# Performance work log

Hardware: AMD Instinct MI355X
Metric: run time of the kernel (lower is better)

Reference implementation:

```python
import jax, jax.numpy as jnp
from jax import lax
import numpy as np

D_IN, D_MODEL, N_CLS, NL = 63, 256, 14, 4
D_INNER, D_STATE, NH, HP, DCONV = 512, 128, 8, 64, 4
CONV_CH = D_INNER + 2 * D_STATE  # 768
PROJ = 2 * D_INNER + 2 * D_STATE + NH  # 1288
EPS = 1e-5


def layernorm(x, w, b):
    mu = jnp.mean(x, -1, keepdims=True)
    var = jnp.mean((x - mu) ** 2, -1, keepdims=True)
    return (x - mu) * lax.rsqrt(var + EPS) * w + b


def mamba2_block(u, inproj_w, conv_w, conv_b, dt_bias, A_log, Dp, norm_w, outp_w):
    B, L, _ = u.shape
    zxbcdt = u @ inproj_w.T  # (B,L,1288)
    z = zxbcdt[..., :D_INNER]
    xBC = zxbcdt[..., D_INNER:D_INNER + CONV_CH]
    dt = zxbcdt[..., D_INNER + CONV_CH:]  # (B,L,NH)
    # depthwise causal conv1d, kernel 4
    xp = jnp.pad(xBC, ((0, 0), (DCONV - 1, 0), (0, 0)))
    conv = conv_b + sum(xp[:, k:k + L, :] * conv_w[k] for k in range(DCONV))
    xBC = jax.nn.silu(conv)
    xs = xBC[..., :D_INNER].reshape(B, L, NH, HP)
    Bm = xBC[..., D_INNER:D_INNER + D_STATE]  # (B,L,N)
    Cm = xBC[..., D_INNER + D_STATE:]
    dt = jax.nn.softplus(dt + dt_bias)  # (B,L,NH)
    A = -jnp.exp(A_log)  # (NH,)
    dA = jnp.exp(dt * A)  # (B,L,NH)
    dtx = dt[..., None] * xs  # (B,L,NH,HP)

    def step(h, inp):
        dA_t, dtx_t, B_t, C_t = inp
        h = h * dA_t[:, :, None, None] + jnp.einsum('bhp,bn->bhpn', dtx_t, B_t)
        y = jnp.einsum('bhpn,bn->bhp', h, C_t)
        return h, y

    h0 = jnp.zeros((B, NH, HP, D_STATE), u.dtype)
    _, ys = lax.scan(step, h0, (dA.transpose(1, 0, 2), dtx.transpose(1, 0, 2, 3),
                                 Bm.transpose(1, 0, 2), Cm.transpose(1, 0, 2)))
    y = ys.transpose(1, 0, 2, 3) + Dp[None, None, :, None] * xs  # (B,L,NH,HP)
    y = y.reshape(B, L, D_INNER)
    g = y * jax.nn.silu(z)  # gated RMSNorm (norm_before_gate=False)
    g = g * lax.rsqrt(jnp.mean(g * g, -1, keepdims=True) + EPS) * norm_w
    return g @ outp_w.T


def setup_inputs() -> dict:
    key = jax.random.key(0)
    ks = jax.random.split(key, 20)
    B, L = 32, 1024
    s = 0.02
    inp = {
        'x': jax.random.normal(ks[0], (B, L, D_IN), jnp.float32),
        'in_w': jax.random.normal(ks[1], (D_MODEL, D_IN)) * s,
        'in_b': jnp.zeros((D_MODEL,)),
        'lnin_w': jnp.ones((D_MODEL,)),
        'lnin_b': jnp.zeros((D_MODEL,)),
        'inproj_w': jax.random.normal(ks[2], (NL, PROJ, D_MODEL)) * s,
        'conv_w': jax.random.normal(ks[3], (NL, DCONV, CONV_CH)) * 0.1,
        'conv_b': jnp.zeros((NL, CONV_CH)),
        'dt_bias': jax.random.uniform(ks[4], (NL, NH), minval=-4.0, maxval=-1.0),
        'A_log': jnp.log(jax.random.uniform(ks[5], (NL, NH), minval=1.0, maxval=16.0)),
        'D': jnp.ones((NL, NH)),
        'norm_w': jnp.ones((NL, D_INNER)),
        'outp_w': jax.random.normal(ks[6], (NL, D_MODEL, D_INNER)) * s,
        'ln_w': jnp.ones((NL, D_MODEL)),
        'ln_b': jnp.zeros((NL, D_MODEL)),
        'head_w': jax.random.normal(ks[7], (N_CLS, D_MODEL)) * s,
        'head_b': jnp.zeros((N_CLS,)),
        'lengths': jax.random.randint(ks[8], (B,), 1, L + 1, dtype=jnp.int32),
    }
    return inp


def reference(x, in_w, in_b, lnin_w, lnin_b, inproj_w, conv_w, conv_b, dt_bias,
              A_log, D, norm_w, outp_w, ln_w, ln_b, head_w, head_b, lengths):
    B, L, _ = x.shape
    h = layernorm(x @ in_w.T + in_b, lnin_w, lnin_b)
    for i in range(NL):
        res = h
        m = mamba2_block(h, inproj_w[i], conv_w[i], conv_b[i], dt_bias[i],
                         A_log[i], D[i], norm_w[i], outp_w[i])
        h = layernorm(m + res, ln_w[i], ln_b[i])
    mask = (jnp.arange(L)[None, :] < lengths[:, None]).astype(h.dtype)[:, :, None]
    pooled = jnp.sum(h * mask, axis=1) / lengths[:, None].astype(h.dtype)
    return pooled @ head_w.T + head_b
```

## Files before the change

### kernel.cpp

```cpp
#include <hip/hip_runtime.h>
#include <math.h>

#define D_IN 63
#define D_MODEL 256
#define N_CLS 14
#define NL 4
#define D_INNER 512
#define D_STATE 128
#define NH 8
#define HP 64
#define DCONV 4
#define CONV_CH 768
#define PROJ 1288
#define XBCDT 776
#define EPS 1e-5f
#define BSZ 32
#define LSEQ 1024
#define NTOK (BSZ*LSEQ)

#define SSEG 4
#define TSEG (LSEQ/SSEG)
#define CT 16

typedef __attribute__((ext_vector_type(8))) short bf16x8;
typedef __attribute__((ext_vector_type(4))) float f32x4;

__device__ __forceinline__ float silu_f(float x) { return x / (1.f + expf(-x)); }

__device__ __forceinline__ unsigned short f2bf(float x) {
    union { float f; unsigned u; } v; v.f = x;
    unsigned r = v.u + 0x7FFFu + ((v.u >> 16) & 1u);
    return (unsigned short)(r >> 16);
}
__device__ __forceinline__ float bf2f(unsigned short h) {
    union { float f; unsigned u; } v; v.u = ((unsigned)h) << 16; return v.f;
}

__device__ __forceinline__ int swz128(int n) {
    int q = n >> 5, i = (n >> 2) & 7, j = n & 3;
    return (q << 5) + (((i + 2 * q) & 7) << 2) + j;
}

__device__ __forceinline__ float2 block_reduce2(float a, float b, float* sred) {
    #pragma unroll
    for (int off = 32; off >= 1; off >>= 1) {
        a += __shfl_xor(a, off);
        b += __shfl_xor(b, off);
    }
    int wid = threadIdx.x >> 6, lane = threadIdx.x & 63;
    if (lane == 0) { sred[wid * 2] = a; sred[wid * 2 + 1] = b; }
    __syncthreads();
    a = sred[0] + sred[2] + sred[4] + sred[6];
    b = sred[1] + sred[3] + sred[5] + sred[7];
    __syncthreads();
    return make_float2(a, b);
}

#define LDKP 40
__global__ __launch_bounds__(256, 2)
void k_gemm_mfma(const float* __restrict__ A, const float* __restrict__ B,
                 float* __restrict__ C, int M, int N, int K) {
    __shared__ unsigned short Ah[128][LDKP], Al[128][LDKP];
    __shared__ unsigned short Bh[128][LDKP], Bl[128][LDKP];
    int n0 = blockIdx.x * 128, m0 = blockIdx.y * 128;
    int tid = threadIdx.x;
    int srow = tid >> 1, sk = (tid & 1) * 16;
    int lane = tid & 63, wave = tid >> 6;
    int wm = (wave >> 1) * 64, wn = (wave & 1) * 64;
    int ln = lane & 15, quad = lane >> 4;
    f32x4 acc[4][4];
    #pragma unroll
    for (int i = 0; i < 4; i++)
        #pragma unroll
        for (int j = 0; j < 4; j++) acc[i][j] = (f32x4){0.f, 0.f, 0.f, 0.f};
    const float* Ap = A + (size_t)(m0 + srow) * K + sk;
    const float* Bp = B + (size_t)(n0 + srow) * K + sk;
    bool bval = (n0 + srow) < N;
    for (int k0 = 0; k0 < K; k0 += 32) {
        float av[16], bv[16];
        #pragma unroll
        for (int i = 0; i < 4; i++) {
            *(float4*)&av[4 * i] = *(const float4*)(Ap + k0 + 4 * i);
            *(float4*)&bv[4 * i] = bval ? *(const float4*)(Bp + k0 + 4 * i)
                                        : make_float4(0.f, 0.f, 0.f, 0.f);
        }
        __syncthreads();
        #pragma unroll
        for (int g = 0; g < 2; g++) {
            unsigned hiA[4], loA[4], hiB[4], loB[4];
            #pragma unroll
            for (int j = 0; j < 4; j++) {
                float a0 = av[8 * g + 2 * j], a1 = av[8 * g + 2 * j + 1];
                unsigned short h0 = f2bf(a0), h1 = f2bf(a1);
                unsigned short l0 = f2bf(a0 - bf2f(h0)), l1 = f2bf(a1 - bf2f(h1));
                hiA[j] = (unsigned)h0 | ((unsigned)h1 << 16);
                loA[j] = (unsigned)l0 | ((unsigned)l1 << 16);
                float b0 = bv[8 * g + 2 * j], b1 = bv[8 * g + 2 * j + 1];
                unsigned short g0 = f2bf(b0), g1 = f2bf(b1);
                unsigned short m0s = f2bf(b0 - bf2f(g0)), m1s = f2bf(b1 - bf2f(g1));
                hiB[j] = (unsigned)g0 | ((unsigned)g1 << 16);
                loB[j] = (unsigned)m0s | ((unsigned)m1s << 16);
            }
            *(uint4*)&Ah[srow][sk + 8 * g] = *(uint4*)hiA;
            *(uint4*)&Al[srow][sk + 8 * g] = *(uint4*)loA;
            *(uint4*)&Bh[srow][sk + 8 * g] = *(uint4*)hiB;
            *(uint4*)&Bl[srow][sk + 8 * g] = *(uint4*)loB;
        }
        __syncthreads();
        bf16x8 fah[4], fal[4], fbh[4], fbl[4];
        #pragma unroll
        for (int t = 0; t < 4; t++) {
            fah[t] = *(const bf16x8*)&Ah[wm + t * 16 + ln][quad * 8];
            fal[t] = *(const bf16x8*)&Al[wm + t * 16 + ln][quad * 8];
            fbh[t] = *(const bf16x8*)&Bh[wn + t * 16 + ln][quad * 8];
            fbl[t] = *(const bf16x8*)&Bl[wn + t * 16 + ln][quad * 8];
        }
        #pragma unroll
        for (int mt = 0; mt < 4; mt++)
            #pragma unroll
            for (int nt = 0; nt < 4; nt++) {
                acc[mt][nt] = __builtin_amdgcn_mfma_f32_16x16x32_bf16(fal[mt], fbh[nt], acc[mt][nt], 0, 0, 0);
                acc[mt][nt] = __builtin_amdgcn_mfma_f32_16x16x32_bf16(fah[mt], fbl[nt], acc[mt][nt], 0, 0, 0);
                acc[mt][nt] = __builtin_amdgcn_mfma_f32_16x16x32_bf16(fah[mt], fbh[nt], acc[mt][nt], 0, 0, 0);
            }
    }
    #pragma unroll
    for (int mt = 0; mt < 4; mt++)
        #pragma unroll
        for (int nt = 0; nt < 4; nt++) {
            int cn = n0 + wn + nt * 16 + ln;
            if (cn < N) {
                #pragma unroll
                for (int r = 0; r < 4; r++) {
                    int cm = m0 + wm + mt * 16 + quad * 4 + r;
                    C[(size_t)cm * N + cn] = acc[mt][nt][r];
                }
            }
        }
}

__global__ __launch_bounds__(256)
void k_pack_x(const float* __restrict__ x, float* __restrict__ xp) {
    size_t idx = (size_t)blockIdx.x * 256 + threadIdx.x;
    int k = (int)(idx & 63);
    size_t m = idx >> 6;
    xp[idx] = (k < D_IN) ? x[m * D_IN + k] : 0.f;
}
__global__ __launch_bounds__(256)
void k_pack_w(const float* __restrict__ w, float* __restrict__ wp) {
    int idx = blockIdx.x * 256 + threadIdx.x;
    int k = idx & 63, n = idx >> 6;
    wp[idx] = (k < D_IN) ? w[n * D_IN + k] : 0.f;
}

__global__ __launch_bounds__(256)
void k_lnio(const float* __restrict__ pre, const float* __restrict__ bias,
            const float* __restrict__ gw, const float* __restrict__ gb,
            float* __restrict__ h) {
    int m = blockIdx.x, o = threadIdx.x;
    __shared__ float sred[8];
    float v = pre[(size_t)m * D_MODEL + o] + bias[o];
    float2 s = block_reduce2(v, v * v, sred);
    float mu = s.x * (1.f / D_MODEL);
    float var = s.y * (1.f / D_MODEL) - mu * mu;
    h[(size_t)m * D_MODEL + o] = (v - mu) * rsqrtf(var + EPS) * gw[o] + gb[o];
}

__global__ __launch_bounds__(256)
void k_conv(const float* __restrict__ xbc, const float* __restrict__ cw,
            const float* __restrict__ cb, const float* __restrict__ dtb,
            float* __restrict__ xs, float* __restrict__ Bm, float* __restrict__ Cm,
            float* __restrict__ dtv) {
    int m = blockIdx.x;
    int l = m & (LSEQ - 1);
    int tid = threadIdx.x;
    #pragma unroll
    for (int it = 0; it < 3; it++) {
        int c = tid + it * 256;
        float acc = cb[c];
        #pragma unroll
        for (int k = 0; k < DCONV; k++) {
            int lp = l - (DCONV - 1) + k;
            if (lp >= 0)
                acc = fmaf(cw[k * CONV_CH + c],
                           xbc[(size_t)(m - (DCONV - 1) + k) * XBCDT + c], acc);
        }
        float v = silu_f(acc);
        if (c < D_INNER) xs[(size_t)m * D_INNER + c] = v;
        else if (c < D_INNER + D_STATE) Bm[(size_t)m * D_STATE + (c - D_INNER)] = v;
        else Cm[(size_t)m * D_STATE + (c - D_INNER - D_STATE)] = v;
    }
    if (tid < NH) {
        float draw = xbc[(size_t)m * XBCDT + CONV_CH + tid] + dtb[tid];
        float dt = draw > 20.f ? draw : log1pf(expf(draw));
        dtv[m * NH + tid] = dt;
    }
}

__global__ __launch_bounds__(256, 4)
void k_scan_seg(const float* __restrict__ xs, const float* __restrict__ Bm,
                const float* __restrict__ Cm, const float* __restrict__ dtv,
                const float* __restrict__ Alog, const float* __restrict__ Dvec,
                float* __restrict__ y, float* __restrict__ F,
                float* __restrict__ cumdA) {
    int blk = blockIdx.x;
    int bh = blk >> 2;
    int seg = blk & (SSEG - 1);
    int b = bh >> 3, hh = bh & 7;
    int tid = threadIdx.x;
    int p = tid >> 2, q = tid & 3;
    int q2 = q << 1;
    __shared__ __align__(16) float sB[CT][D_STATE];
    __shared__ __align__(16) float sC[CT][D_STATE];
    __shared__ __align__(16) float sX[CT][HP];
    __shared__ float sdt[CT], sdA[CT];
    float hst[32];
    #pragma unroll
    for (int i = 0; i < 32; i++) hst[i] = 0.f;
    float Dh = Dvec[hh];
    float Ah = -expf(Alog[hh]);
    float c_run = 1.f;
    const size_t base = (size_t)b * LSEQ + (size_t)seg * TSEG;
    int col = tid & 127, half = tid >> 7;
    int sw = swz128(col);
    int xc = tid & 63, xh = tid >> 6;

    for (int c0 = 0; c0 < TSEG; c0 += CT) {
        #pragma unroll
        for (int u = 0; u < 8; u++) {
            int s = 2 * u + half;
            size_t m = base + c0 + s;
            sB[s][sw] = Bm[m * D_STATE + col];
            sC[s][sw] = Cm[m * D_STATE + col];
        }
        #pragma unroll
        for (int u = 0; u < 4; u++) {
            int s = 4 * u + xh;
            size_t m = base + c0 + s;
            sX[s][xc] = xs[m * D_INNER + hh * HP + xc];
        }
        if (tid < CT) {
            size_t m = base + c0 + tid;
            float dtl = dtv[m * NH + hh];
            sdt[tid] = dtl;
            sdA[tid] = expf(dtl * Ah);
        }
        __syncthreads();
        if (tid == 0) {
            float cc = c_run;
            for (int s = 0; s < CT; s++) {
                cc *= sdA[s];
                cumdA[(base + c0 + s) * NH + hh] = cc;
            }
            c_run = cc;
        }
        #pragma unroll 1
        for (int s = 0; s < CT; s++) {
            float dtl = sdt[s], dAl = sdA[s];
            float xv = sX[s][p];
            float tmp = dtl * xv;
            float yp = 0.f;
            #pragma unroll
            for (int i = 0; i < 8; i++) {
                int off = (q << 5) + (((i + q2) & 7) << 2);
                float4 bvv = *(const float4*)&sB[s][off];
                float4 cvv = *(const float4*)&sC[s][off];
                hst[4*i+0] = fmaf(hst[4*i+0], dAl, tmp * bvv.x); yp = fmaf(hst[4*i+0], cvv.x, yp);
                hst[4*i+1] = fmaf(hst[4*i+1], dAl, tmp * bvv.y); yp = fmaf(hst[4*i+1], cvv.y, yp);
                hst[4*i+2] = fmaf(hst[4*i+2], dAl, tmp * bvv.z); yp = fmaf(hst[4*i+2], cvv.z, yp);
                hst[4*i+3] = fmaf(hst[4*i+3], dAl, tmp * bvv.w); yp = fmaf(hst[4*i+3], cvv.w, yp);
            }
            yp += __shfl_xor(yp, 1);
            yp += __shfl_xor(yp, 2);
            if (q == 0) y[(base + c0 + s) * D_INNER + hh * HP + p] = fmaf(Dh, xv, yp);
        }
        __syncthreads();
    }
    float* Fp = F + (((size_t)bh * SSEG + seg) * HP + p) * D_STATE + (q << 5);
    #pragma unroll
    for (int i = 0; i < 8; i++)
        *(float4*)(Fp + 4 * i) = make_float4(hst[4*i], hst[4*i+1], hst[4*i+2], hst[4*i+3]);
}

__global__ __launch_bounds__(256)
void k_seg_comb(float* __restrict__ F, const float* __restrict__ cumdA) {
    int bh = blockIdx.x, b = bh >> 3, hh = bh & 7;
    int tid = threadIdx.x, p = tid >> 2, q = tid & 3;
    float h[32];
    #pragma unroll
    for (int i = 0; i < 32; i++) h[i] = 0.f;
    for (int s = 0; s < SSEG - 1; s++) {
        float P = cumdA[((size_t)b * LSEQ + (size_t)(s + 1) * TSEG - 1) * NH + hh];
        float* Fp = F + (((size_t)bh * SSEG + s) * HP + p) * D_STATE + (q << 5);
        #pragma unroll
        for (int i = 0; i < 8; i++) {
            float4 f = *(const float4*)(Fp + 4 * i);
            h[4*i+0] = fmaf(h[4*i+0], P, f.x);
            h[4*i+1] = fmaf(h[4*i+1], P, f.y);
            h[4*i+2] = fmaf(h[4*i+2], P, f.z);
            h[4*i+3] = fmaf(h[4*i+3], P, f.w);
        }
        #pragma unroll
        for (int i = 0; i < 8; i++)
            *(float4*)(Fp + 4 * i) = make_float4(h[4*i], h[4*i+1], h[4*i+2], h[4*i+3]);
    }
}

__global__ __launch_bounds__(256, 4)
void k_seg_fix(const float* __restrict__ Cm, const float* __restrict__ cumdA,
               const float* __restrict__ F, float* __restrict__ y) {
    int blk = blockIdx.x;
    int bh = blk / (SSEG - 1);
    int seg = blk - bh * (SSEG - 1) + 1;
    int b = bh >> 3, hh = bh & 7;
    int tid = threadIdx.x, p = tid >> 2, q = tid & 3;
    int q2 = q << 1;
    float hin[32];
    const float* Fp = F + (((size_t)bh * SSEG + (seg - 1)) * HP + p) * D_STATE + (q << 5);
    #pragma unroll
    for (int i = 0; i < 8; i++) {
        float4 f = *(const float4*)(Fp + 4 * i);
        hin[4*i+0] = f.x; hin[4*i+1] = f.y; hin[4*i+2] = f.z; hin[4*i+3] = f.w;
    }
    __shared__ __align__(16) float sC[CT][D_STATE];
    __shared__ float scd[CT];
    const size_t base = (size_t)b * LSEQ + (size_t)seg * TSEG;
    int col = tid & 127, half = tid >> 7;
    int sw = swz128(col);
    for (int c0 = 0; c0 < TSEG; c0 += CT) {
        #pragma unroll
        for (int u = 0; u < 8; u++) {
            int s = 2 * u + half;
            sC[s][sw] = Cm[(base + c0 + s) * D_STATE + col];
        }
        if (tid < CT) scd[tid] = cumdA[(base + c0 + tid) * NH + hh];
        __syncthreads();
        #pragma unroll 1
        for (int s = 0; s < CT; s++) {
            float yp = 0.f;
            #pragma unroll
            for (int i = 0; i < 8; i++) {
                int off = (q << 5) + (((i + q2) & 7) << 2);
                float4 cvv = *(const float4*)&sC[s][off];
                yp = fmaf(hin[4*i+0], cvv.x, yp);
                yp = fmaf(hin[4*i+1], cvv.y, yp);
                yp = fmaf(hin[4*i+2], cvv.z, yp);
                yp = fmaf(hin[4*i+3], cvv.w, yp);
            }
            yp += __shfl_xor(yp, 1);
            yp += __shfl_xor(yp, 2);
            if (q == 0) {
                size_t idx = (base + c0 + s) * D_INNER + hh * HP + p;
                y[idx] += scd[s] * yp;
            }
        }
        __syncthreads();
    }
}

__global__ __launch_bounds__(256)
void k_gate(float* __restrict__ y, const float* __restrict__ zbuf,
            const float* __restrict__ nw) {
    int m = blockIdx.x, tid = threadIdx.x;
    __shared__ float sred[8];
    float g[2];
    #pragma unroll
    for (int j = 0; j < 2; j++) {
        int d = tid + j * 256;
        float z = zbuf[(size_t)m * D_INNER + d];
        g[j] = y[(size_t)m * D_INNER + d] * silu_f(z);
    }
    float2 s = block_reduce2(g[0] * g[0] + g[1] * g[1], 0.f, sred);
    float r = rsqrtf(s.x * (1.f / D_INNER) + EPS);
    #pragma unroll
    for (int j = 0; j < 2; j++) {
        int d = tid + j * 256;
        y[(size_t)m * D_INNER + d] = g[j] * r * nw[d];
    }
}

__global__ __launch_bounds__(256)
void k_addln(const float* __restrict__ mo, float* __restrict__ h,
             const float* __restrict__ w, const float* __restrict__ bias) {
    int m = blockIdx.x, o = threadIdx.x;
    __shared__ float sred[8];
    float v = mo[(size_t)m * D_MODEL + o] + h[(size_t)m * D_MODEL + o];
    float2 s = block_reduce2(v, v * v, sred);
    float mu = s.x * (1.f / D_MODEL);
    float var = s.y * (1.f / D_MODEL) - mu * mu;
    h[(size_t)m * D_MODEL + o] = (v - mu) * rsqrtf(var + EPS) * w[o] + bias[o];
}

__global__ __launch_bounds__(256)
void k_pool_head(const float* __restrict__ h, const int* __restrict__ len,
                 const float* __restrict__ hw, const float* __restrict__ hb,
                 float* __restrict__ out) {
    int b = blockIdx.x, d = threadIdx.x;
    __shared__ float sp[D_MODEL];
    int Lb = len[b];
    float acc = 0.f;
    for (int l = 0; l < Lb; l++) acc += h[((size_t)b * LSEQ + l) * D_MODEL + d];
    sp[d] = acc / (float)Lb;
    __syncthreads();
    if (d < N_CLS) {
        float o = hb[d];
        const float* wr = hw + (size_t)d * D_MODEL;
        #pragma unroll 8
        for (int k = 0; k < D_MODEL; k++) o = fmaf(sp[k], wr[k], o);
        out[b * N_CLS + d] = o;
    }
}

extern "C" void kernel_launch(void* const* d_in, const int* in_sizes, int n_in,
                              void* d_out, int out_size, void* d_ws, size_t ws_size,
                              hipStream_t stream) {
    const float* x      = (const float*)d_in[0];
    const float* in_w   = (const float*)d_in[1];
    const float* in_b   = (const float*)d_in[2];
    const float* lnin_w = (const float*)d_in[3];
    const float* lnin_b = (const float*)d_in[4];
    const float* inproj = (const float*)d_in[5];
    const float* conv_w = (const float*)d_in[6];
    const float* conv_b = (const float*)d_in[7];
    const float* dt_bias= (const float*)d_in[8];
    const float* A_log  = (const float*)d_in[9];
    const float* Dv     = (const float*)d_in[10];
    const float* norm_w = (const float*)d_in[11];
    const float* outp_w = (const float*)d_in[12];
    const float* ln_w   = (const float*)d_in[13];
    const float* ln_b   = (const float*)d_in[14];
    const float* head_w = (const float*)d_in[15];
    const float* head_b = (const float*)d_in[16];
    const int*   lengths= (const int*)d_in[17];
    float* out = (float*)d_out;

    float* ws    = (float*)d_ws;
    float* h     = ws;
    float* buf1  = h    + (size_t)NTOK * D_MODEL;
    float* xs    = buf1 + (size_t)NTOK * XBCDT;
    float* Bm    = xs   + (size_t)NTOK * D_INNER;
    float* Cm    = Bm   + (size_t)NTOK * D_STATE;
    float* dtv   = Cm   + (size_t)NTOK * D_STATE;
    float* cumdA = dtv  + (size_t)NTOK * NH;
    float* zbuf  = buf1;
    float* F     = buf1 + (size_t)NTOK * D_INNER;
    float* mo    = Bm;
    float* xp    = buf1;
    float* pre   = buf1 + (size_t)NTOK * 64;
    float* wp    = Bm;

    k_pack_x<<<NTOK * 64 / 256, 256, 0, stream>>>(x, xp);
    k_pack_w<<<64, 256, 0, stream>>>(in_w, wp);
    {
        dim3 g(D_MODEL / 128, NTOK / 128);
        k_gemm_mfma<<<g, 256, 0, stream>>>(xp, wp, pre, NTOK, D_MODEL, 64);
    }
    k_lnio<<<NTOK, 256, 0, stream>>>(pre, in_b, lnin_w, lnin_b, h);

    for (int i = 0; i < NL; i++) {
        const float* W = inproj + (size_t)i * PROJ * D_MODEL;
        dim3 g1a((XBCDT + 127) / 128, NTOK / 128);
        k_gemm_mfma<<<g1a, 256, 0, stream>>>(h, W + (size_t)D_INNER * D_MODEL,
                                             buf1, NTOK, XBCDT, D_MODEL);
        k_conv<<<NTOK, 256, 0, stream>>>(buf1, conv_w + i * DCONV * CONV_CH,
                                         conv_b + i * CONV_CH, dt_bias + i * NH,
                                         xs, Bm, Cm, dtv);
        dim3 g1b(D_INNER / 128, NTOK / 128);
        k_gemm_mfma<<<g1b, 256, 0, stream>>>(h, W, zbuf, NTOK, D_INNER, D_MODEL);
        k_scan_seg<<<BSZ * NH * SSEG, 256, 0, stream>>>(xs, Bm, Cm, dtv,
                                                        A_log + i * NH, Dv + i * NH,
                                                        xs, F, cumdA);
        k_seg_comb<<<BSZ * NH, 256, 0, stream>>>(F, cumdA);
        k_seg_fix<<<BSZ * NH * (SSEG - 1), 256, 0, stream>>>(Cm, cumdA, F, xs);
        k_gate<<<NTOK, 256, 0, stream>>>(xs, zbuf, norm_w + i * D_INNER);
        dim3 g2(D_MODEL / 128, NTOK / 128);
        k_gemm_mfma<<<g2, 256, 0, stream>>>(xs, outp_w + (size_t)i * D_MODEL * D_INNER,
                                            mo, NTOK, D_MODEL, D_INNER);
        k_addln<<<NTOK, 256, 0, stream>>>(mo, h, ln_w + i * D_MODEL, ln_b + i * D_MODEL);
    }

    k_pool_head<<<BSZ, 256, 0, stream>>>(h, lengths, head_w, head_b, out);
}
```

Before: 3.227 ms.

## Pre-split weights to bf16 hi/lo, rescale scan recurrence, fold segment combine into fix

Adds a one-time kernel that splits all weights into bf16 hi/lo pairs, so the GEMMs only split the activation operand on the fly. Rewrites the scan inner loop to drop the per-element decay multiply by keeping a running cumulative decay and its reciprocal, renormalising every RS steps or when the decay underflows. Removes the separate segment-combine kernel by having each seg_fix block accumulate the earlier segments' final states itself. The risks are numerical drift from the reciprocal scaling, extra redundant combine work in seg_fix, and dependence on workspace size for the packed path.

```diff
diff --git a/kernel.cpp b/kernel.cpp
--- a/kernel.cpp
+++ b/kernel.cpp
@@ -21,6 +21,20 @@
 #define SSEG 4
 #define TSEG (LSEQ/SSEG)
 #define CT 16
+#define RS 8
+
+#define S_IN   16384
+#define S_IP   1318912
+#define S_OP   524288
+#define IN_HI  0
+#define IN_LO  16384
+#define IP_HI  32768
+#define IP_LO  (32768 + S_IP)
+#define OP_HI  (32768 + 2*S_IP)
+#define OP_LO  (OP_HI + S_OP)
+#define TOTPK  (S_IN + S_IP + S_OP)
+#define WS_BASE ((size_t)NTOK * 1816)
+#define WS_NEED ((WS_BASE + (size_t)TOTPK) * 4)
 
 typedef __attribute__((ext_vector_type(8))) short bf16x8;
 typedef __attribute__((ext_vector_type(4))) float f32x4;
@@ -56,7 +70,114 @@
     return make_float2(a, b);
 }
 
+__global__ __launch_bounds__(256)
+void k_pack_weights(const float* __restrict__ in_w, const float* __restrict__ inproj,
+                    const float* __restrict__ outp, unsigned short* __restrict__ WP) {
+    int idx = blockIdx.x * 256 + threadIdx.x;
+    float v; int hi_off, lo_off;
+    if (idx < S_IN) {
+        int n = idx >> 6, k = idx & 63;
+        v = (k < D_IN) ? in_w[n * D_IN + k] : 0.f;
+        hi_off = IN_HI + idx; lo_off = IN_LO + idx;
+    } else if (idx < S_IN + S_IP) {
+        int j = idx - S_IN;
+        v = inproj[j];
+        hi_off = IP_HI + j; lo_off = IP_LO + j;
+    } else {
+        int j = idx - S_IN - S_IP;
+        v = outp[j];
+        hi_off = OP_HI + j; lo_off = OP_LO + j;
+    }
+    unsigned short h = f2bf(v);
+    unsigned short l = f2bf(v - bf2f(h));
+    WP[hi_off] = h; WP[lo_off] = l;
+}
+
 #define LDKP 40
+__global__ __launch_bounds__(256, 2)
+void k_gemm_as(const float* __restrict__ A, const unsigned short* __restrict__ Bhg,
+               const unsigned short* __restrict__ Blg, float* __restrict__ C,
+               int M, int N, int K) {
+    __shared__ unsigned short Ah[128][LDKP], Al[128][LDKP];
+    __shared__ unsigned short Bh[128][LDKP], Bl[128][LDKP];
+    int n0 = blockIdx.x * 128, m0 = blockIdx.y * 128;
+    int tid = threadIdx.x;
+    int srow = tid >> 1, sk = (tid & 1) * 16;
+    int lane = tid & 63, wave = tid >> 6;
+    int wm = (wave >> 1) * 64, wn = (wave & 1) * 64;
+    int ln = lane & 15, quad = lane >> 4;
+    f32x4 acc[4][4];
+    #pragma unroll
+    for (int i = 0; i < 4; i++)
+        #pragma unroll
+        for (int j = 0; j < 4; j++) acc[i][j] = (f32x4){0.f, 0.f, 0.f, 0.f};
+    const float* Ap = A + (size_t)(m0 + srow) * K + sk;
+    const unsigned short* Bhp = Bhg + (size_t)(n0 + srow) * K + sk;
+    const unsigned short* Blp = Blg + (size_t)(n0 + srow) * K + sk;
+    bool bval = (n0 + srow) < N;
+    uint4 z4 = make_uint4(0u, 0u, 0u, 0u);
+    for (int k0 = 0; k0 < K; k0 += 32) {
+        float av[16];
+        #pragma unroll
+        for (int i = 0; i < 4; i++)
+            *(float4*)&av[4 * i] = *(const float4*)(Ap + k0 + 4 * i);
+        uint4 bh0 = bval ? *(const uint4*)(Bhp + k0) : z4;
+        uint4 bh1 = bval ? *(const uint4*)(Bhp + k0 + 8) : z4;
+        uint4 bl0 = bval ? *(const uint4*)(Blp + k0) : z4;
+        uint4 bl1 = bval ? *(const uint4*)(Blp + k0 + 8) : z4;
+        unsigned hp[8], lp[8];
+        #pragma unroll
+        for (int j = 0; j < 8; j++) {
+            float a0 = av[2 * j], a1 = av[2 * j + 1];
+            unsigned u0 = __float_as_uint(a0), u1 = __float_as_uint(a1);
+            unsigned h0 = u0 & 0xFFFF0000u, h1 = u1 & 0xFFFF0000u;
+            float r0 = a0 - __uint_as_float(h0);
+            float r1 = a1 - __uint_as_float(h1);
+            hp[j] = (u0 >> 16) | h1;
+            lp[j] = (__float_as_uint(r0) >> 16) | (__float_as_uint(r1) & 0xFFFF0000u);
+        }
+        __syncthreads();
+        *(uint4*)&Ah[srow][sk]     = *(uint4*)&hp[0];
+        *(uint4*)&Ah[srow][sk + 8] = *(uint4*)&hp[4];
+        *(uint4*)&Al[srow][sk]     = *(uint4*)&lp[0];
+        *(uint4*)&Al[srow][sk + 8] = *(uint4*)&lp[4];
+        *(uint4*)&Bh[srow][sk]     = bh0;
+        *(uint4*)&Bh[srow][sk + 8] = bh1;
+        *(uint4*)&Bl[srow][sk]     = bl0;
+        *(uint4*)&Bl[srow][sk + 8] = bl1;
+        __syncthreads();
+        bf16x8 fah[4], fal[4], fbh[4], fbl[4];
+        #pragma unroll
+        for (int t = 0; t < 4; t++) {
+            fah[t] = *(const bf16x8*)&Ah[wm + t * 16 + ln][quad * 8];
+            fal[t] = *(const bf16x8*)&Al[wm + t * 16 + ln][quad * 8];
+            fbh[t] = *(const bf16x8*)&Bh[wn + t * 16 + ln][quad * 8];
+            fbl[t] = *(const bf16x8*)&Bl[wn + t * 16 + ln][quad * 8];
+        }
+        #pragma unroll
+        for (int mt = 0; mt < 4; mt++)
+            #pragma unroll
+            for (int nt = 0; nt < 4; nt++) {
+                acc[mt][nt] = __builtin_amdgcn_mfma_f32_16x16x32_bf16(fal[mt], fbh[nt], acc[mt][nt], 0, 0, 0);
+                acc[mt][nt] = __builtin_amdgcn_mfma_f32_16x16x32_bf16(fah[mt], fbl[nt], acc[mt][nt], 0, 0, 0);
+                acc[mt][nt] = __builtin_amdgcn_mfma_f32_16x16x32_bf16(fah[mt], fbh[nt], acc[mt][nt], 0, 0, 0);
+            }
+    }
+    #pragma unroll
+    for (int mt = 0; mt < 4; mt++)
+        #pragma unroll
+        for (int nt = 0; nt < 4; nt++) {
+            int cn = n0 + wn + nt * 16 + ln;
+            if (cn < N) {
+                #pragma unroll
+                for (int r = 0; r < 4; r++) {
+                    int cm = m0 + wm + mt * 16 + quad * 4 + r;
+                    C[(size_t)cm * N + cn] = acc[mt][nt][r];
+                }
+            }
+        }
+}
+
 __global__ __launch_bounds__(256, 2)
 void k_gemm_mfma(const float* __restrict__ A, const float* __restrict__ B,
                  float* __restrict__ C, int M, int N, int K) {
@@ -210,15 +331,14 @@
     int tid = threadIdx.x;
     int p = tid >> 2, q = tid & 3;
     int q2 = q << 1;
-    __shared__ __align__(16) float sB[CT][D_STATE];
-    __shared__ __align__(16) float sC[CT][D_STATE];
+    __shared__ __align__(16) float sBC[2 * CT * 128];
     __shared__ __align__(16) float sX[CT][HP];
-    __shared__ float sdt[CT], sdA[CT];
+    __shared__ float sdt[CT], sdA[CT], srdA[CT];
     float hst[32];
     #pragma unroll
     for (int i = 0; i < 32; i++) hst[i] = 0.f;
     float Dh = Dvec[hh];
-    float Ah = -expf(Alog[hh]);
+    float Ahv = -expf(Alog[hh]);
     float c_run = 1.f;
     const size_t base = (size_t)b * LSEQ + (size_t)seg * TSEG;
     int col = tid & 127, half = tid >> 7;
@@ -230,79 +350,73 @@
         for (int u = 0; u < 8; u++) {
             int s = 2 * u + half;
             size_t m = base + c0 + s;
-            sB[s][sw] = Bm[m * D_STATE + col];
-            sC[s][sw] = Cm[m * D_STATE + col];
+            sBC[s * 128 + sw] = Bm[m * D_STATE + col];
+            sBC[(CT + s) * 128 + sw] = Cm[m * D_STATE + col];
         }
         #pragma unroll
         for (int u = 0; u < 4; u++) {
             int s = 4 * u + xh;
-            size_t m = base + c0 + s;
-            sX[s][xc] = xs[m * D_INNER + hh * HP + xc];
+            sX[s][xc] = xs[(base + c0 + s) * D_INNER + hh * HP + xc];
         }
         if (tid < CT) {
-            size_t m = base + c0 + tid;
-            float dtl = dtv[m * NH + hh];
+            float dtl = dtv[(base + c0 + tid) * NH + hh];
+            float e = fmaxf(dtl * Ahv, -37.f);
             sdt[tid] = dtl;
-            sdA[tid] = expf(dtl * Ah);
+            sdA[tid] = expf(e);
+            srdA[tid] = expf(-e);
         }
         __syncthreads();
         if (tid == 0) {
-            float cc = c_run;
+            float cg = c_run;
             for (int s = 0; s < CT; s++) {
-                cc *= sdA[s];
-                cumdA[(base + c0 + s) * NH + hh] = cc;
-            }
-            c_run = cc;
-        }
-        #pragma unroll 1
+                cg *= sdA[s];
+                cumdA[(base + c0 + s) * NH + hh] = cg;
+            }
+            c_run = cg;
+        }
+        float cc = 1.f, rc = 1.f;
+        #pragma unroll
         for (int s = 0; s < CT; s++) {
-            float dtl = sdt[s], dAl = sdA[s];
+            float dAl = sdA[s], dtl = sdt[s];
+            float ccn = cc * dAl;
+            if (ccn < 1e-18f) {
+                #pragma unroll
+                for (int i = 0; i < 32; i++) hst[i] *= cc;
+                rc = srdA[s];
+                ccn = dAl;
+            } else {
+                rc *= srdA[s];
+            }
+            cc = ccn;
             float xv = sX[s][p];
-            float tmp = dtl * xv;
+            float tmp = dtl * xv * rc;
             float yp = 0.f;
             #pragma unroll
             for (int i = 0; i < 8; i++) {
                 int off = (q << 5) + (((i + q2) & 7) << 2);
-                float4 bvv = *(const float4*)&sB[s][off];
-                float4 cvv = *(const float4*)&sC[s][off];
-                hst[4*i+0] = fmaf(hst[4*i+0], dAl, tmp * bvv.x); yp = fmaf(hst[4*i+0], cvv.x, yp);
-                hst[4*i+1] = fmaf(hst[4*i+1], dAl, tmp * bvv.y); yp = fmaf(hst[4*i+1], cvv.y, yp);
-                hst[4*i+2] = fmaf(hst[4*i+2], dAl, tmp * bvv.z); yp = fmaf(hst[4*i+2], cvv.z, yp);
-                hst[4*i+3] = fmaf(hst[4*i+3], dAl, tmp * bvv.w); yp = fmaf(hst[4*i+3], cvv.w, yp);
+                float4 bv = *(const float4*)&sBC[s * 128 + off];
+                float4 cv = *(const float4*)&sBC[(CT + s) * 128 + off];
+                hst[4*i+0] = fmaf(tmp, bv.x, hst[4*i+0]); yp = fmaf(hst[4*i+0], cv.x, yp);
+                hst[4*i+1] = fmaf(tmp, bv.y, hst[4*i+1]); yp = fmaf(hst[4*i+1], cv.y, yp);
+                hst[4*i+2] = fmaf(tmp, bv.z, hst[4*i+2]); yp = fmaf(hst[4*i+2], cv.z, yp);
+                hst[4*i+3] = fmaf(tmp, bv.w, hst[4*i+3]); yp = fmaf(hst[4*i+3], cv.w, yp);
             }
             yp += __shfl_xor(yp, 1);
             yp += __shfl_xor(yp, 2);
-            if (q == 0) y[(base + c0 + s) * D_INNER + hh * HP + p] = fmaf(Dh, xv, yp);
-        }
-        __syncthreads();
-    }
-    float* Fp = F + (((size_t)bh * SSEG + seg) * HP + p) * D_STATE + (q << 5);
-    #pragma unroll
-    for (int i = 0; i < 8; i++)
-        *(float4*)(Fp + 4 * i) = make_float4(hst[4*i], hst[4*i+1], hst[4*i+2], hst[4*i+3]);
-}
-
-__global__ __launch_bounds__(256)
-void k_seg_comb(float* __restrict__ F, const float* __restrict__ cumdA) {
-    int bh = blockIdx.x, b = bh >> 3, hh = bh & 7;
-    int tid = threadIdx.x, p = tid >> 2, q = tid & 3;
-    float h[32];
-    #pragma unroll
-    for (int i = 0; i < 32; i++) h[i] = 0.f;
-    for (int s = 0; s < SSEG - 1; s++) {
-        float P = cumdA[((size_t)b * LSEQ + (size_t)(s + 1) * TSEG - 1) * NH + hh];
-        float* Fp = F + (((size_t)bh * SSEG + s) * HP + p) * D_STATE + (q << 5);
-        #pragma unroll
-        for (int i = 0; i < 8; i++) {
-            float4 f = *(const float4*)(Fp + 4 * i);
-            h[4*i+0] = fmaf(h[4*i+0], P, f.x);
-            h[4*i+1] = fmaf(h[4*i+1], P, f.y);
-            h[4*i+2] = fmaf(h[4*i+2], P, f.z);
-            h[4*i+3] = fmaf(h[4*i+3], P, f.w);
-        }
+            if (q == 0) y[(base + c0 + s) * D_INNER + hh * HP + p] = fmaf(Dh, xv, cc * yp);
+            if ((s & (RS - 1)) == RS - 1) {
+                #pragma unroll
+                for (int i = 0; i < 32; i++) hst[i] *= cc;
+                cc = 1.f; rc = 1.f;
+            }
+        }
+        __syncthreads();
+    }
+    if (seg < SSEG - 1) {
+        float* Fp = F + (((size_t)bh * (SSEG - 1) + seg) * HP + p) * D_STATE + (q << 5);
         #pragma unroll
         for (int i = 0; i < 8; i++)
-            *(float4*)(Fp + 4 * i) = make_float4(h[4*i], h[4*i+1], h[4*i+2], h[4*i+3]);
+            *(float4*)(Fp + 4 * i) = make_float4(hst[4*i], hst[4*i+1], hst[4*i+2], hst[4*i+3]);
     }
 }
 
@@ -316,11 +430,19 @@
     int tid = threadIdx.x, p = tid >> 2, q = tid & 3;
     int q2 = q << 1;
     float hin[32];
-    const float* Fp = F + (((size_t)bh * SSEG + (seg - 1)) * HP + p) * D_STATE + (q << 5);
-    #pragma unroll
-    for (int i = 0; i < 8; i++) {
-        float4 f = *(const float4*)(Fp + 4 * i);
-        hin[4*i+0] = f.x; hin[4*i+1] = f.y; hin[4*i+2] = f.z; hin[4*i+3] = f.w;
+    #pragma unroll
+    for (int i = 0; i < 32; i++) hin[i] = 0.f;
+    for (int s = 0; s < seg; s++) {
+        float P = cumdA[((size_t)b * LSEQ + (size_t)(s + 1) * TSEG - 1) * NH + hh];
+        const float* Fp = F + (((size_t)bh * (SSEG - 1) + s) * HP + p) * D_STATE + (q << 5);
+        #pragma unroll
+        for (int i = 0; i < 8; i++) {
+            float4 f = *(const float4*)(Fp + 4 * i);
+            hin[4*i+0] = fmaf(hin[4*i+0], P, f.x);
+            hin[4*i+1] = fmaf(hin[4*i+1], P, f.y);
+            hin[4*i+2] = fmaf(hin[4*i+2], P, f.z);
+            hin[4*i+3] = fmaf(hin[4*i+3], P, f.w);
+        }
     }
     __shared__ __align__(16) float sC[CT][D_STATE];
     __shared__ float scd[CT];
@@ -447,36 +569,62 @@
     float* mo    = Bm;
     float* xp    = buf1;
     float* pre   = buf1 + (size_t)NTOK * 64;
-    float* wp    = Bm;
-
-    k_pack_x<<<NTOK * 64 / 256, 256, 0, stream>>>(x, xp);
-    k_pack_w<<<64, 256, 0, stream>>>(in_w, wp);
-    {
-        dim3 g(D_MODEL / 128, NTOK / 128);
-        k_gemm_mfma<<<g, 256, 0, stream>>>(xp, wp, pre, NTOK, D_MODEL, 64);
-    }
-    k_lnio<<<NTOK, 256, 0, stream>>>(pre, in_b, lnin_w, lnin_b, h);
-
-    for (int i = 0; i < NL; i++) {
-        const float* W = inproj + (size_t)i * PROJ * D_MODEL;
-        dim3 g1a((XBCDT + 127) / 128, NTOK / 128);
-        k_gemm_mfma<<<g1a, 256, 0, stream>>>(h, W + (size_t)D_INNER * D_MODEL,
-                                             buf1, NTOK, XBCDT, D_MODEL);
-        k_conv<<<NTOK, 256, 0, stream>>>(buf1, conv_w + i * DCONV * CONV_CH,
-                                         conv_b + i * CONV_CH, dt_bias + i * NH,
-                                         xs, Bm, Cm, dtv);
-        dim3 g1b(D_INNER / 128, NTOK / 128);
-        k_gemm_mfma<<<g1b, 256, 0, stream>>>(h, W, zbuf, NTOK, D_INNER, D_MODEL);
-        k_scan_seg<<<BSZ * NH * SSEG, 256, 0, stream>>>(xs, Bm, Cm, dtv,
-                                                        A_log + i * NH, Dv + i * NH,
-                                                        xs, F, cumdA);
-        k_seg_comb<<<BSZ * NH, 256, 0, stream>>>(F, cumdA);
-        k_seg_fix<<<BSZ * NH * (SSEG - 1), 256, 0, stream>>>(Cm, cumdA, F, xs);
-        k_gate<<<NTOK, 256, 0, stream>>>(xs, zbuf, norm_w + i * D_INNER);
-        dim3 g2(D_MODEL / 128, NTOK / 128);
-        k_gemm_mfma<<<g2, 256, 0, stream>>>(xs, outp_w + (size_t)i * D_MODEL * D_INNER,
-                                            mo, NTOK, D_MODEL, D_INNER);
-        k_addln<<<NTOK, 256, 0, stream>>>(mo, h, ln_w + i * D_MODEL, ln_b + i * D_MODEL);
+    unsigned short* WP = (unsigned short*)(ws + WS_BASE);
+    bool use_pk = (ws_size >= WS_NEED);
+
+    dim3 gIO(D_MODEL / 128, NTOK / 128);
+    dim3 g1a((XBCDT + 127) / 128, NTOK / 128);
+    dim3 g1b(D_INNER / 128, NTOK / 128);
+
+    if (use_pk) {
+        k_pack_weights<<<TOTPK / 256, 256, 0, stream>>>(in_w, inproj, outp_w, WP);
+        k_pack_x<<<NTOK * 64 / 256, 256, 0, stream>>>(x, xp);
+        k_gemm_as<<<gIO, 256, 0, stream>>>(xp, WP + IN_HI, WP + IN_LO, pre,
+                                           NTOK, D_MODEL, 64);
+        k_lnio<<<NTOK, 256, 0, stream>>>(pre, in_b, lnin_w, lnin_b, h);
+        for (int i = 0; i < NL; i++) {
+            const unsigned short* iph = WP + IP_HI + (size_t)i * PROJ * D_MODEL;
+            const unsigned short* ipl = WP + IP_LO + (size_t)i * PROJ * D_MODEL;
+            k_gemm_as<<<g1a, 256, 0, stream>>>(h, iph + (size_t)D_INNER * D_MODEL,
+                                               ipl + (size_t)D_INNER * D_MODEL,
+                                               buf1, NTOK, XBCDT, D_MODEL);
+            k_conv<<<NTOK, 256, 0, stream>>>(buf1, conv_w + i * DCONV * CONV_CH,
+                                             conv_b + i * CONV_CH, dt_bias + i * NH,
+                                             xs, Bm, Cm, dtv);
+            k_gemm_as<<<g1b, 256, 0, stream>>>(h, iph, ipl, zbuf, NTOK, D_INNER, D_MODEL);
+            k_scan_seg<<<BSZ * NH * SSEG, 256, 0, stream>>>(xs, Bm, Cm, dtv,
+                                                            A_log + i * NH, Dv + i * NH,
+                                                            xs, F, cumdA);
+            k_seg_fix<<<BSZ * NH * (SSEG - 1), 256, 0, stream>>>(Cm, cumdA, F, xs);
+            k_gate<<<NTOK, 256, 0, stream>>>(xs, zbuf, norm_w + i * D_INNER);
+            k_gemm_as<<<gIO, 256, 0, stream>>>(xs, WP + OP_HI + (size_t)i * D_MODEL * D_INNER,
+                                               WP + OP_LO + (size_t)i * D_MODEL * D_INNER,
+                                               mo, NTOK, D_MODEL, D_INNER);
+            k_addln<<<NTOK, 256, 0, stream>>>(mo, h, ln_w + i * D_MODEL, ln_b + i * D_MODEL);
+        }
+    } else {
+        float* wp = Bm;
+        k_pack_x<<<NTOK * 64 / 256, 256, 0, stream>>>(x, xp);
+        k_pack_w<<<64, 256, 0, stream>>>(in_w, wp);
+        k_gemm_mfma<<<gIO, 256, 0, stream>>>(xp, wp, pre, NTOK, D_MODEL, 64);
+        k_lnio<<<NTOK, 256, 0, stream>>>(pre, in_b, lnin_w, lnin_b, h);
+        for (int i = 0; i < NL; i++) {
+            const float* W = inproj + (size_t)i * PROJ * D_MODEL;
+            k_gemm_mfma<<<g1a, 256, 0, stream>>>(h, W + (size_t)D_INNER * D_MODEL,
+                                                 buf1, NTOK, XBCDT, D_MODEL);
+            k_conv<<<NTOK, 256, 0, stream>>>(buf1, conv_w + i * DCONV * CONV_CH,
+                                             conv_b + i * CONV_CH, dt_bias + i * NH,
+                                             xs, Bm, Cm, dtv);
+            k_gemm_mfma<<<g1b, 256, 0, stream>>>(h, W, zbuf, NTOK, D_INNER, D_MODEL);
+            k_scan_seg<<<BSZ * NH * SSEG, 256, 0, stream>>>(xs, Bm, Cm, dtv,
+                                                            A_log + i * NH, Dv + i * NH,
+                                                            xs, F, cumdA);
+            k_seg_fix<<<BSZ * NH * (SSEG - 1), 256, 0, stream>>>(Cm, cumdA, F, xs);
+            k_gate<<<NTOK, 256, 0, stream>>>(xs, zbuf, norm_w + i * D_INNER);
+            k_gemm_mfma<<<gIO, 256, 0, stream>>>(xs, outp_w + (size_t)i * D_MODEL * D_INNER,
+                                                 mo, NTOK, D_MODEL, D_INNER);
+            k_addln<<<NTOK, 256, 0, stream>>>(mo, h, ln_w + i * D_MODEL, ln_b + i * D_MODEL);
+        }
     }
 
     k_pool_head<<<BSZ, 256, 0, stream>>>(h, lengths, head_w, head_b, out);
```

Result: faster. 3.014 ms (-6.6%).
